# Performance work log

Measured on AMD Instinct MI355X. Metric: run time of the kernel, lower is better.

Reference implementation:

```python
import jax, jax.numpy as jnp
import numpy as np

B, C, H, W = 64, 512, 28, 28
NL = 4  # number of (layer, attention) pairs iterated over


def setup_inputs() -> dict:
    key = jax.random.key(0)
    ks = jax.random.split(key, 6)
    n = lambda k, sh: jax.random.normal(k, sh, dtype=jnp.float32) * 0.05
    return {
        "x": n(ks[0], (B, C, H, W)),
        "w_ih_l1": n(ks[1], (C // 16, C)),
        "b_ih_l1": jnp.zeros((C // 16,), jnp.float32),
        "w_ih_l2": n(ks[2], (3 * C, C // 16)),
        "b_ih_l2": jnp.zeros((3 * C,), jnp.float32),
        "w_hh_l1": n(ks[3], (C // 16, C)),
        "b_hh_l1": jnp.zeros((C // 16,), jnp.float32),
        "w_hh_l2": n(ks[4], (3 * C, C // 16)),
        "b_hh_l2": jnp.zeros((3 * C,), jnp.float32),
        "dw_kernel": n(ks[5], (C, 1, 3, 3)),  # depthwise 3x3, groups=C, no bias
        "num_layers": NL,
    }


def reference(x, w_ih_l1, b_ih_l1, w_ih_l2, b_ih_l2,
              w_hh_l1, b_hh_l1, w_hh_l2, b_hh_l2, dw_kernel, num_layers):
    # DSU cell (nlayers=1): bottleneck MLP gates, LSTM-style state update.
    def cell(inp, hx, cx):
        g_i = jnp.dot(jax.nn.relu(jnp.dot(inp, w_ih_l1.T) + b_ih_l1), w_ih_l2.T) + b_ih_l2
        g_h = jnp.dot(jax.nn.relu(jnp.dot(hx, w_hh_l1.T) + b_hh_l1), w_hh_l2.T) + b_hh_l2
        i_g, f_g, c_g = jnp.split(g_i + g_h, 3, axis=-1)
        ncx = jax.nn.sigmoid(f_g) * cx + jax.nn.sigmoid(i_g) * jnp.tanh(c_g)
        return jax.nn.sigmoid(ncx), ncx

    b, c = x.shape[0], x.shape[1]
    ht = jnp.zeros((b, c), x.dtype)
    ct = jnp.zeros((b, c), x.dtype)

    for _ in range(int(num_layers)):
        org = x  # layer stub: layer(x) -> (x, x)
        # recurrent SE path on pooled features
        seq = jnp.mean(x, axis=(2, 3))  # [B, C]
        ht, ct = cell(seq, ht, ct)
        # second DSU call: original indexes hidden[0][0] on a [B,C] tensor,
        # i.e. uses batch element 0 as hx/cx (broadcast) -- replicated faithfully.
        y_in = jnp.mean(org, axis=(2, 3))
        out_h, _ = cell(y_in, ht[0], ct[0])  # [B, C]
        # depthwise 3x3 conv on org
        re = jax.lax.conv_general_dilated(
            org, dw_kernel, window_strides=(1, 1), padding="SAME",
            feature_group_count=c, dimension_numbers=("NCHW", "OIHW", "NCHW"))
        org = org * out_h[:, :, None, None] + re
        x = x + org  # attention stub: attention(x, org) -> x + org
    return x
```

## Files before the change

kernel.cpp:

```cpp
#include <hip/hip_runtime.h>


#define HW 784
#define F4 196
#define CC 512
#define BB 64
#define NP 32768
#define TS 31

__device__ __forceinline__ float sigm(float x) { return 1.f / (1.f + __expf(-x)); }

#define STENCIL(src, py, px4, w0,w1,w2,w3,w4,w5,w6,w7,w8, y0,y1,y2,y3) do { \
    const float* r0 = &(src)[(py) * TS + (px4) * 4]; \
    const float* r1 = r0 + TS; \
    const float* r2 = r0 + 2 * TS; \
    float a0=r0[0],a1=r0[1],a2=r0[2],a3=r0[3],a4=r0[4],a5=r0[5]; \
    float b0=r1[0],b1=r1[1],b2=r1[2],b3=r1[3],b4=r1[4],b5=r1[5]; \
    float c0=r2[0],c1=r2[1],c2=r2[2],c3=r2[3],c4=r2[4],c5=r2[5]; \
    y0 = a0*w0+a1*w1+a2*w2 + b0*w3+b1*w4+b2*w5 + c0*w6+c1*w7+c2*w8; \
    y1 = a1*w0+a2*w1+a3*w2 + b1*w3+b2*w4+b3*w5 + c1*w6+c2*w7+c3*w8; \
    y2 = a2*w0+a3*w1+a4*w2 + b2*w3+b3*w4+b4*w5 + c2*w6+c3*w7+c4*w8; \
    y3 = a3*w0+a4*w1+a5*w2 + b3*w3+b4*w4+b5*w5 + c3*w6+c4*w7+c5*w8; \
} while (0)

#define ZERO_HALO(tile) do { \
    if (t < 30) (tile)[t] = 0.f; \
    else if (t < 60) (tile)[29 * TS + (t - 30)] = 0.f; \
    else if (t < 88) (tile)[(t - 59) * TS] = 0.f; \
    else if (t < 116) (tile)[(t - 87) * TS + 29] = 0.f; \
} while (0)

__global__ void __launch_bounds__(256) wj_kernel(const float* __restrict__ dwk,
                                                 float* __restrict__ W) {
    __shared__ float tA[30 * TS], tB[30 * TS];
    __shared__ float s_w[9];
    int c = blockIdx.x, t = threadIdx.x;
    ZERO_HALO(tA); ZERO_HALO(tB);
    if (t < 9) s_w[t] = dwk[c * 9 + 8 - t];
    int py = t / 7, px4 = t - py * 7;
    if (t < F4) {
        float* d = &tA[(py + 1) * TS + px4 * 4 + 1];
        d[0] = d[1] = d[2] = d[3] = 1.f;
    }
    __syncthreads();
    float w0=s_w[0],w1=s_w[1],w2=s_w[2],w3=s_w[3],w4=s_w[4],w5=s_w[5],w6=s_w[6],w7=s_w[7],w8=s_w[8];
    float* src = tA; float* dst = tB;
    for (int it = 1; it <= 3; ++it) {
        if (t < F4) {
            float y0, y1, y2, y3;
            STENCIL(src, py, px4, w0,w1,w2,w3,w4,w5,w6,w7,w8, y0,y1,y2,y3);
            float* d = &dst[(py + 1) * TS + px4 * 4 + 1];
            d[0]=y0; d[1]=y1; d[2]=y2; d[3]=y3;
            ((float4*)(W + ((size_t)(it - 1) * CC + c) * HW))[t] = make_float4(y0,y1,y2,y3);
        }
        __syncthreads();
        float* tmp = src; src = dst; dst = tmp;
    }
}

__global__ void __launch_bounds__(256) stats_kernel(const float* __restrict__ x,
                                                    const float* __restrict__ W,
                                                    float* __restrict__ mu) {
    int wave = threadIdx.x >> 6, lane = threadIdx.x & 63;
    int p = blockIdx.x * 4 + wave;
    int c = p & 511;
    const float4* xv = (const float4*)(x + (size_t)p * HW);
    const float4* w1 = (const float4*)(W + (size_t)c * HW);
    const float4* w2 = (const float4*)(W + ((size_t)CC + c) * HW);
    const float4* w3 = (const float4*)(W + ((size_t)2 * CC + c) * HW);
    float s0 = 0.f, s1 = 0.f, s2 = 0.f, s3 = 0.f;
    for (int j = lane; j < F4; j += 64) {
        float4 v = xv[j], a = w1[j], b = w2[j], d = w3[j];
        s0 += v.x + v.y + v.z + v.w;
        s1 += v.x*a.x + v.y*a.y + v.z*a.z + v.w*a.w;
        s2 += v.x*b.x + v.y*b.y + v.z*b.z + v.w*b.w;
        s3 += v.x*d.x + v.y*d.y + v.z*d.z + v.w*d.w;
    }
    #pragma unroll
    for (int off = 32; off > 0; off >>= 1) {
        s0 += __shfl_down(s0, off, 64);
        s1 += __shfl_down(s1, off, 64);
        s2 += __shfl_down(s2, off, 64);
        s3 += __shfl_down(s3, off, 64);
    }
    if (lane == 0) {
        mu[p]          = s0 * (1.f / 784.f);
        mu[NP + p]     = s1 * (1.f / 784.f);
        mu[2 * NP + p] = s2 * (1.f / 784.f);
        mu[3 * NP + p] = s3 * (1.f / 784.f);
    }
}

__global__ void __launch_bounds__(512) cell_kernel(
        const float* __restrict__ mu, float* __restrict__ coef,
        const float* __restrict__ w_ih1, const float* __restrict__ b_ih1,
        const float* __restrict__ w_ih2, const float* __restrict__ b_ih2,
        const float* __restrict__ w_hh1, const float* __restrict__ b_hh1,
        const float* __restrict__ w_hh2, const float* __restrict__ b_hh2,
        float* __restrict__ G_i, float* __restrict__ ct,
        float* __restrict__ g_hpre, float* __restrict__ g_h2c,
        float* __restrict__ ct0c, int k) {
    __shared__ __align__(16) float s_in[CC];
    __shared__ float s_hid[32];
    __shared__ float s_hid2[32];
    __shared__ float s_g[1536];
    const int b = blockIdx.x, t = threadIdx.x;
    const int p = b * CC + t;

    float c0, c1, c2, c3;
    if (k == 0) {
        c0 = 1.f; c1 = c2 = c3 = 0.f;
        if (t < 32) s_hid2[t] = fmaxf(b_hh1[t], 0.f);
    } else {
        c0 = coef[p]; c1 = coef[NP + p]; c2 = coef[2 * NP + p]; c3 = coef[3 * NP + p];
        const float* g  = G_i + b * 1536;
        const float* gh = g_h2c + (size_t)(k - 1) * 1536;
        float ig = g[t] + gh[t];
        float fg = g[CC + t] + gh[CC + t];
        float cg = g[2 * CC + t] + gh[2 * CC + t];
        float nc = sigm(fg) * ct0c[(k - 1) * CC + t] + sigm(ig) * tanhf(cg);
        float A = 1.f + sigm(nc);
        c3 = A * c3 + c2; c2 = A * c2 + c1; c1 = A * c1 + c0; c0 = A * c0;
    }
    coef[p] = c0; coef[NP + p] = c1; coef[2 * NP + p] = c2; coef[3 * NP + p] = c3;
    s_in[t] = c0 * mu[p] + c1 * mu[NP + p] + c2 * mu[2 * NP + p] + c3 * mu[3 * NP + p];
    __syncthreads();

    {
        int o = t >> 4, q = t & 15;
        const float4* wv4 = (const float4*)(w_ih1 + o * CC) + q * 8;
        const float4* in4 = (const float4*)s_in + q * 8;
        float acc = 0.f;
        #pragma unroll
        for (int j = 0; j < 8; ++j) {
            float4 w = wv4[j], xv = in4[j];
            acc += xv.x*w.x + xv.y*w.y + xv.z*w.z + xv.w*w.w;
        }
        acc += __shfl_down(acc, 8, 64);
        acc += __shfl_down(acc, 4, 64);
        acc += __shfl_down(acc, 2, 64);
        acc += __shfl_down(acc, 1, 64);
        if (q == 0) s_hid[o] = fmaxf(acc + b_ih1[o], 0.f);
    }
    __syncthreads();

    for (int o = t; o < 1536; o += 512) {
        const float4* wv4 = (const float4*)(w_ih2 + o * 32);
        float acc = 0.f;
        #pragma unroll
        for (int j = 0; j < 8; ++j) {
            float4 w = wv4[j];
            acc += s_hid[4*j]*w.x + s_hid[4*j+1]*w.y + s_hid[4*j+2]*w.z + s_hid[4*j+3]*w.w;
        }
        float gi = acc + b_ih2[o];
        G_i[b * 1536 + o] = gi;
        float gh;
        if (k == 0) {
            const float4* hv4 = (const float4*)(w_hh2 + o * 32);
            float a2 = 0.f;
            #pragma unroll
            for (int j = 0; j < 8; ++j) {
                float4 w = hv4[j];
                a2 += s_hid2[4*j]*w.x + s_hid2[4*j+1]*w.y + s_hid2[4*j+2]*w.z + s_hid2[4*j+3]*w.w;
            }
            gh = a2 + b_hh2[o];
        } else {
            gh = g_hpre[b * 1536 + o];
        }
        s_g[o] = gi + gh;
    }
    __syncthreads();

    {
        float ctold = (k == 0) ? 0.f : ct[p];
        float nc = sigm(s_g[CC + t]) * ctold + sigm(s_g[t]) * tanhf(s_g[2 * CC + t]);
        ct[p] = nc;
        if (b == 0) ct0c[k * CC + t] = nc;
        s_in[t] = sigm(nc);
    }
    __syncthreads();

    {
        int o = t >> 4, q = t & 15;
        const float4* wv4 = (const float4*)(w_hh1 + o * CC) + q * 8;
        const float4* in4 = (const float4*)s_in + q * 8;
        float acc = 0.f;
        #pragma unroll
        for (int j = 0; j < 8; ++j) {
            float4 w = wv4[j], xv = in4[j];
            acc += xv.x*w.x + xv.y*w.y + xv.z*w.z + xv.w*w.w;
        }
        acc += __shfl_down(acc, 8, 64);
        acc += __shfl_down(acc, 4, 64);
        acc += __shfl_down(acc, 2, 64);
        acc += __shfl_down(acc, 1, 64);
        if (q == 0) s_hid[o] = fmaxf(acc + b_hh1[o], 0.f);
    }
    __syncthreads();

    for (int o = t; o < 1536; o += 512) {
        const float4* wv4 = (const float4*)(w_hh2 + o * 32);
        float acc = 0.f;
        #pragma unroll
        for (int j = 0; j < 8; ++j) {
            float4 w = wv4[j];
            acc += s_hid[4*j]*w.x + s_hid[4*j+1]*w.y + s_hid[4*j+2]*w.z + s_hid[4*j+3]*w.w;
        }
        acc += b_hh2[o];
        g_hpre[b * 1536 + o] = acc;
        if (b == 0) g_h2c[(size_t)k * 1536 + o] = acc;
    }
}

__global__ void __launch_bounds__(256) mega_kernel(
        const float* __restrict__ x, float* __restrict__ out,
        const float* __restrict__ G_i, const float* __restrict__ g_h2c,
        const float* __restrict__ ct0c, const float* __restrict__ coef,
        const float* __restrict__ dwk) {
    __shared__ float tA[30 * TS], tB[30 * TS];
    __shared__ float s_w[9];
    __shared__ float s_e[5];
    int p = blockIdx.x, t = threadIdx.x;
    int b = p >> 9, c = p & 511;
    ZERO_HALO(tA); ZERO_HALO(tB);
    if (t < 9) s_w[t] = dwk[c * 9 + t];
    if (t == 255) {
        const float* g  = G_i + b * 1536;
        const float* gh = g_h2c + 3 * 1536;
        float ig = g[c] + gh[c];
        float fg = g[CC + c] + gh[CC + c];
        float cg = g[2 * CC + c] + gh[2 * CC + c];
        float nc = sigm(fg) * ct0c[3 * CC + c] + sigm(ig) * tanhf(cg);
        float A = 1.f + sigm(nc);
        float c0 = coef[p], c1 = coef[NP + p], c2 = coef[2 * NP + p], c3 = coef[3 * NP + p];
        s_e[4] = c3;
        s_e[3] = A * c3 + c2;
        s_e[2] = A * c2 + c1;
        s_e[1] = A * c1 + c0;
        s_e[0] = A * c0;
    }
    int py = t / 7, px4 = t - py * 7;
    float4 v = make_float4(0.f, 0.f, 0.f, 0.f);
    if (t < F4) {
        v = ((const float4*)(x + (size_t)p * HW))[t];
        float* d = &tA[(py + 1) * TS + px4 * 4 + 1];
        d[0] = v.x; d[1] = v.y; d[2] = v.z; d[3] = v.w;
    }
    __syncthreads();
    float w0=s_w[0],w1=s_w[1],w2=s_w[2],w3=s_w[3],w4=s_w[4],w5=s_w[5],w6=s_w[6],w7=s_w[7],w8=s_w[8];
    float e0=s_e[0], e1=s_e[1], e2=s_e[2], e3=s_e[3], e4=s_e[4];
    float acc0 = e0 * v.x, acc1 = e0 * v.y, acc2 = e0 * v.z, acc3 = e0 * v.w;
    float* src = tA; float* dst = tB;
    #pragma unroll
    for (int it = 1; it <= 4; ++it) {
        float e = (it == 1) ? e1 : (it == 2) ? e2 : (it == 3) ? e3 : e4;
        if (t < F4) {
            float y0, y1, y2, y3;
            STENCIL(src, py, px4, w0,w1,w2,w3,w4,w5,w6,w7,w8, y0,y1,y2,y3);
            acc0 += e * y0; acc1 += e * y1; acc2 += e * y2; acc3 += e * y3;
            float* d = &dst[(py + 1) * TS + px4 * 4 + 1];
            d[0]=y0; d[1]=y1; d[2]=y2; d[3]=y3;
        }
        __syncthreads();
        float* tmp = src; src = dst; dst = tmp;
    }
    if (t < F4)
        ((float4*)(out + (size_t)p * HW))[t] = make_float4(acc0, acc1, acc2, acc3);
}

extern "C" void kernel_launch(void* const* d_in, const int* in_sizes, int n_in,
                              void* d_out, int out_size, void* d_ws, size_t ws_size,
                              hipStream_t stream) {
    const float* x_in  = (const float*)d_in[0];
    const float* w_ih1 = (const float*)d_in[1];
    const float* b_ih1 = (const float*)d_in[2];
    const float* w_ih2 = (const float*)d_in[3];
    const float* b_ih2 = (const float*)d_in[4];
    const float* w_hh1 = (const float*)d_in[5];
    const float* b_hh1 = (const float*)d_in[6];
    const float* w_hh2 = (const float*)d_in[7];
    const float* b_hh2 = (const float*)d_in[8];
    const float* dwk   = (const float*)d_in[9];
    float* out = (float*)d_out;
    char* ws = (char*)d_ws;

    float* mu    = (float*)(ws + 0);
    float* coef  = (float*)(ws + 524288);
    float* G_i   = (float*)(ws + 1048576);
    float* ct    = (float*)(ws + 1441792);
    float* g_hpre= (float*)(ws + 1572864);
    float* g_h2c = (float*)(ws + 1966080);
    float* ct0c  = (float*)(ws + 1990656);
    float* Wbuf  = (float*)(ws + 1998848);

    wj_kernel<<<512, 256, 0, stream>>>(dwk, Wbuf);
    stats_kernel<<<8192, 256, 0, stream>>>(x_in, Wbuf, mu);
    for (int k = 0; k < 4; ++k)
        cell_kernel<<<BB, 512, 0, stream>>>(mu, coef, w_ih1, b_ih1, w_ih2, b_ih2,
                                            w_hh1, b_hh1, w_hh2, b_hh2,
                                            G_i, ct, g_hpre, g_h2c, ct0c, k);
    mega_kernel<<<NP, 256, 0, stream>>>(x_in, out, G_i, g_h2c, ct0c, coef, dwk);
}
```

Before: 374.9 us.

## Restructure stencil kernel to column-per-lane with 8 planes per block

The final polynomial-of-conv kernel now handles 8 (b,c) planes per 256-thread block, two per wavefront. Each lane keeps one 28-element image column in registers and swaps neighbour columns through wavefront-private LDS, with no block-level barriers. The polynomial is evaluated in Horner form (e4, e3, ... applied as nested stencils plus e*x), so the separate accumulator goes away. This targets the idle-thread and __syncthreads overhead of the one-plane-per-block design, which left 60 of 256 threads idle and synced every iteration. The cost is high register pressure from four 28-float arrays, and correctness depends on implicit wavefront-synchronous LDS ordering with only compiler barriers.

```diff
diff --git a/kernel.cpp b/kernel.cpp
--- a/kernel.cpp
+++ b/kernel.cpp
@@ -212,60 +212,140 @@
     }
 }
 
+__device__ __forceinline__ void rdcol(const float4* C4, int cc, float (&D)[28]) {
+    const float4* s4 = C4 + cc * 9;
+    #pragma unroll
+    for (int j = 0; j < 7; ++j) {
+        float4 v = s4[j];
+        D[4*j] = v.x; D[4*j+1] = v.y; D[4*j+2] = v.z; D[4*j+3] = v.w;
+    }
+}
+__device__ __forceinline__ void zcol(float (&D)[28]) {
+    #pragma unroll
+    for (int r = 0; r < 28; ++r) D[r] = 0.f;
+}
+__device__ __forceinline__ void wrcol(float4* C4, int cc, const float (&S)[28]) {
+    #pragma unroll
+    for (int j = 0; j < 7; ++j)
+        C4[cc * 9 + j] = make_float4(S[4*j], S[4*j+1], S[4*j+2], S[4*j+3]);
+}
+
 __global__ void __launch_bounds__(256) mega_kernel(
         const float* __restrict__ x, float* __restrict__ out,
         const float* __restrict__ G_i, const float* __restrict__ g_h2c,
         const float* __restrict__ ct0c, const float* __restrict__ coef,
         const float* __restrict__ dwk) {
-    __shared__ float tA[30 * TS], tB[30 * TS];
-    __shared__ float s_w[9];
-    __shared__ float s_e[5];
-    int p = blockIdx.x, t = threadIdx.x;
-    int b = p >> 9, c = p & 511;
-    ZERO_HALO(tA); ZERO_HALO(tB);
-    if (t < 9) s_w[t] = dwk[c * 9 + t];
-    if (t == 255) {
-        const float* g  = G_i + b * 1536;
-        const float* gh = g_h2c + 3 * 1536;
-        float ig = g[c] + gh[c];
-        float fg = g[CC + c] + gh[CC + c];
-        float cg = g[2 * CC + c] + gh[2 * CC + c];
-        float nc = sigm(fg) * ct0c[3 * CC + c] + sigm(ig) * tanhf(cg);
-        float A = 1.f + sigm(nc);
-        float c0 = coef[p], c1 = coef[NP + p], c2 = coef[2 * NP + p], c3 = coef[3 * NP + p];
-        s_e[4] = c3;
-        s_e[3] = A * c3 + c2;
-        s_e[2] = A * c2 + c1;
-        s_e[1] = A * c1 + c0;
-        s_e[0] = A * c0;
-    }
-    int py = t / 7, px4 = t - py * 7;
-    float4 v = make_float4(0.f, 0.f, 0.f, 0.f);
-    if (t < F4) {
-        v = ((const float4*)(x + (size_t)p * HW))[t];
-        float* d = &tA[(py + 1) * TS + px4 * 4 + 1];
-        d[0] = v.x; d[1] = v.y; d[2] = v.z; d[3] = v.w;
-    }
-    __syncthreads();
-    float w0=s_w[0],w1=s_w[1],w2=s_w[2],w3=s_w[3],w4=s_w[4],w5=s_w[5],w6=s_w[6],w7=s_w[7],w8=s_w[8];
-    float e0=s_e[0], e1=s_e[1], e2=s_e[2], e3=s_e[3], e4=s_e[4];
-    float acc0 = e0 * v.x, acc1 = e0 * v.y, acc2 = e0 * v.z, acc3 = e0 * v.w;
-    float* src = tA; float* dst = tB;
-    #pragma unroll
-    for (int it = 1; it <= 4; ++it) {
-        float e = (it == 1) ? e1 : (it == 2) ? e2 : (it == 3) ? e3 : e4;
-        if (t < F4) {
-            float y0, y1, y2, y3;
-            STENCIL(src, py, px4, w0,w1,w2,w3,w4,w5,w6,w7,w8, y0,y1,y2,y3);
-            acc0 += e * y0; acc1 += e * y1; acc2 += e * y2; acc3 += e * y3;
-            float* d = &dst[(py + 1) * TS + px4 * 4 + 1];
-            d[0]=y0; d[1]=y1; d[2]=y2; d[3]=y3;
-        }
-        __syncthreads();
-        float* tmp = src; src = dst; dst = tmp;
-    }
-    if (t < F4)
-        ((float4*)(out + (size_t)p * HW))[t] = make_float4(acc0, acc1, acc2, acc3);
+    __shared__ float lds[8 * 1008];
+    const int t = threadIdx.x;
+    const int w = t >> 6, lane = t & 63;
+    const int h = lane >> 5, c = lane & 31;
+    const int pl = 2 * w + h;
+    const int p = blockIdx.x * 8 + pl;
+    const int b = p >> 9, ch = p & 511;
+    const bool act = (c < 28);
+
+    {
+        const float4* xg = (const float4*)(x + (size_t)(blockIdx.x * 8 + 2 * w) * HW);
+        float4* L = (float4*)(lds + 2 * w * 1008);
+        #pragma unroll
+        for (int i0 = 0; i0 < 7; ++i0) {
+            int i = i0 * 64 + lane;
+            if (i < 392) {
+                int q = i / 196, rem = i - q * 196;
+                int row = rem / 7, c4 = rem - row * 7;
+                L[q * 252 + row * 7 + c4] = xg[i];
+            }
+        }
+    }
+    asm volatile("" ::: "memory");
+
+    const float* g  = G_i + b * 1536;
+    const float* gh = g_h2c + 3 * 1536;
+    float ig = g[ch] + gh[ch];
+    float fg = g[CC + ch] + gh[CC + ch];
+    float cg = g[2 * CC + ch] + gh[2 * CC + ch];
+    float ncv = sigm(fg) * ct0c[3 * CC + ch] + sigm(ig) * tanhf(cg);
+    float A = 1.f + sigm(ncv);
+    float k0 = coef[p], k1 = coef[NP + p], k2 = coef[2 * NP + p], k3 = coef[3 * NP + p];
+    float e4 = k3, e3 = A*k3 + k2, e2 = A*k2 + k1, e1 = A*k1 + k0, e0 = A*k0;
+    float w0 = dwk[ch*9+0], w1 = dwk[ch*9+1], w2 = dwk[ch*9+2];
+    float w3 = dwk[ch*9+3], w4 = dwk[ch*9+4], w5 = dwk[ch*9+5];
+    float w6 = dwk[ch*9+6], w7 = dwk[ch*9+7], w8 = dwk[ch*9+8];
+
+    float* P = lds + pl * 1008;
+    float4* C4 = (float4*)lds + pl * 252;
+
+    float xr[28], tt[28], l[28], rr[28];
+
+    if (act) {
+        #pragma unroll
+        for (int r = 0; r < 28; ++r) xr[r] = P[r * 28 + c];
+    }
+    asm volatile("" ::: "memory");
+    if (act) wrcol(C4, c, xr);
+    asm volatile("" ::: "memory");
+
+    if (act) {
+        if (c > 0) rdcol(C4, c - 1, l); else zcol(l);
+        if (c < 27) rdcol(C4, c + 1, rr); else zcol(rr);
+        #pragma unroll
+        for (int r = 0; r < 28; ++r) {
+            float tm1 = (r > 0) ? xr[r-1] : 0.f, tp1 = (r < 27) ? xr[r+1] : 0.f;
+            float lm1 = (r > 0) ? l[r-1]  : 0.f, lp1 = (r < 27) ? l[r+1]  : 0.f;
+            float rm1 = (r > 0) ? rr[r-1] : 0.f, rp1 = (r < 27) ? rr[r+1] : 0.f;
+            float tap = w0*lm1 + w1*tm1 + w2*rm1 + w3*l[r] + w4*xr[r] + w5*rr[r]
+                      + w6*lp1 + w7*tp1 + w8*rp1;
+            tt[r] = e3 * xr[r] + e4 * tap;
+        }
+    }
+    asm volatile("" ::: "memory");
+    if (act) wrcol(C4, c, tt);
+    asm volatile("" ::: "memory");
+
+    #pragma unroll
+    for (int it = 2; it <= 4; ++it) {
+        float e = (it == 2) ? e2 : (it == 3) ? e1 : e0;
+        if (act) {
+            if (c > 0) rdcol(C4, c - 1, l); else zcol(l);
+            if (c < 27) rdcol(C4, c + 1, rr); else zcol(rr);
+            float pm1 = 0.f;
+            #pragma unroll
+            for (int r = 0; r < 28; ++r) {
+                float cur = tt[r];
+                float tp1 = (r < 27) ? tt[r+1] : 0.f;
+                float lm1 = (r > 0) ? l[r-1]  : 0.f, lp1 = (r < 27) ? l[r+1]  : 0.f;
+                float rm1 = (r > 0) ? rr[r-1] : 0.f, rp1 = (r < 27) ? rr[r+1] : 0.f;
+                float tap = w0*lm1 + w1*pm1 + w2*rm1 + w3*l[r] + w4*cur + w5*rr[r]
+                          + w6*lp1 + w7*tp1 + w8*rp1;
+                tt[r] = e * xr[r] + tap;
+                pm1 = cur;
+            }
+        }
+        asm volatile("" ::: "memory");
+        if (it < 4) {
+            if (act) wrcol(C4, c, tt);
+            asm volatile("" ::: "memory");
+        }
+    }
+
+    if (act) {
+        #pragma unroll
+        for (int r = 0; r < 28; ++r) P[r * 28 + c] = tt[r];
+    }
+    asm volatile("" ::: "memory");
+    {
+        float4* og = (float4*)(out + (size_t)(blockIdx.x * 8 + 2 * w) * HW);
+        const float4* L = (const float4*)(lds + 2 * w * 1008);
+        #pragma unroll
+        for (int i0 = 0; i0 < 7; ++i0) {
+            int i = i0 * 64 + lane;
+            if (i < 392) {
+                int q = i / 196, rem = i - q * 196;
+                int row = rem / 7, c4 = rem - row * 7;
+                og[i] = L[q * 252 + row * 7 + c4];
+            }
+        }
+    }
 }
 
 extern "C" void kernel_launch(void* const* d_in, const int* in_sizes, int n_in,
@@ -299,5 +379,5 @@
         cell_kernel<<<BB, 512, 0, stream>>>(mu, coef, w_ih1, b_ih1, w_ih2, b_ih2,
                                             w_hh1, b_hh1, w_hh2, b_hh2,
                                             G_i, ct, g_hpre, g_h2c, ct0c, k);
-    mega_kernel<<<NP, 256, 0, stream>>>(x_in, out, G_i, g_h2c, ct0c, coef, dwk);
-}
+    mega_kernel<<<4096, 256, 0, stream>>>(x_in, out, G_i, g_h2c, ct0c, coef, dwk);
+}
```

Result: faster. 337.5 us (-10.0%).
